# Kernel tuning notes

Hardware: AMD Instinct MI355X
Metric: run time of the kernel (lower is better)

The kernel has to match this reference:

```python
import jax, jax.numpy as jnp
import numpy as np

SEQDIM = 512      # hidden-state dim of h
EMBED_DIM = 512   # attention embedding dim
VFEAT_DIM = 384   # visual feature channels (must equal VFEAT_LEN for the broadcast in the original code)
VFEAT_LEN = 384   # number of visual regions


def setup_inputs() -> dict:
    key = jax.random.key(0)
    k_h, k_v, k_wh, k_wv, k_wg = jax.random.split(key, 5)
    h = jax.random.normal(k_h, (SEQDIM, 1), dtype=jnp.float32)
    v = jax.random.normal(k_v, (VFEAT_DIM, VFEAT_LEN), dtype=jnp.float32)
    wh = jax.random.normal(k_wh, (VFEAT_LEN, EMBED_DIM), dtype=jnp.float32) * 0.05
    wv = jax.random.normal(k_wv, (EMBED_DIM, VFEAT_DIM), dtype=jnp.float32) * 0.05
    wg = jax.random.normal(k_wg, (EMBED_DIM, SEQDIM), dtype=jnp.float32) * 0.05
    return {"h": h, "v": v, "wh": wh, "wv": wv, "wg": wg}


def reference(h, v, wh, wv, wg):
    # s = W_v V + (W_g h_t) 1^T  -> (embed_dim, vfeat_len)
    s = jnp.matmul(wv, v) + jnp.matmul(wg, h)  # (E, L) + (E, 1) broadcasts == outer product with ones row
    # z = w_h tanh(s)            -> (vfeat_len, vfeat_len)
    z = jnp.matmul(wh, jnp.tanh(s))
    alpha = jax.nn.softmax(z, axis=-1)
    # v (D, L) * alpha[..., None] (L, L, 1) -> broadcast to (L, D, L) with D == L
    weighted_avg = v * alpha[..., None]
    return weighted_avg
```

## Files before the change

kernel.cpp:

```cpp
#include <hip/hip_runtime.h>
#include <hip/hip_bf16.h>

#define SDIM 512
#define EDIM 512
#define LDIM 384
#define DDIM 384

typedef __attribute__((ext_vector_type(4))) float float4v;

__global__ __launch_bounds__(256) void k_tanh_s(
    const float* __restrict__ h, const float* __restrict__ v,
    const float* __restrict__ wv, const float* __restrict__ wg,
    float* __restrict__ t)
{
    const int e0  = blockIdx.x * 2;
    const int tid = threadIdx.x;
    __shared__ float wvs[2 * DDIM];
    __shared__ float red[2][2];

    {
        const int row  = tid >> 7;
        const int l128 = tid & 127;
        float acc = 0.f;
        for (int k = l128; k < SDIM; k += 128)
            acc += wg[(e0 + row) * SDIM + k] * h[k];
        for (int off = 32; off > 0; off >>= 1)
            acc += __shfl_down(acc, off, 64);
        if ((tid & 63) == 0) red[row][(tid >> 6) & 1] = acc;
    }

    for (int k = tid; k < 2 * DDIM; k += 256)
        wvs[k] = wv[e0 * DDIM + k];
    __syncthreads();

    const float gh0 = red[0][0] + red[0][1];
    const float gh1 = red[1][0] + red[1][1];

    for (int l = tid; l < LDIM; l += 256) {
        float a0 = 0.f, a1 = 0.f, b0 = 0.f, b1 = 0.f;
        const float* vp = v + l;
        #pragma unroll 8
        for (int k = 0; k < DDIM; k += 2) {
            const float v0 = vp[k * LDIM];
            const float v1 = vp[(k + 1) * LDIM];
            a0 += wvs[k]        * v0;
            a1 += wvs[k + 1]    * v1;
            b0 += wvs[DDIM + k]     * v0;
            b1 += wvs[DDIM + k + 1] * v1;
        }
        t[e0 * LDIM + l]       = tanhf((a0 + a1) + gh0);
        t[(e0 + 1) * LDIM + l] = tanhf((b0 + b1) + gh1);
    }
}

__global__ __launch_bounds__(256) void k_softmax(
    const float* __restrict__ wh, const float* __restrict__ t,
    float* __restrict__ alpha)
{
    const int r0  = blockIdx.x * 2;
    const int tid = threadIdx.x;
    __shared__ float whs[2 * EDIM];
    __shared__ float zr[2][LDIM];
    __shared__ float redm[2][2];
    __shared__ float reds[2][2];

    for (int e = tid; e < 2 * EDIM; e += 256)
        whs[e] = wh[r0 * EDIM + e];
    __syncthreads();

    for (int c = tid; c < LDIM; c += 256) {
        float z00 = 0.f, z01 = 0.f, z10 = 0.f, z11 = 0.f;
        #pragma unroll 8
        for (int e = 0; e < EDIM; e += 2) {
            const float t0 = t[e * LDIM + c];
            const float t1 = t[(e + 1) * LDIM + c];
            z00 += whs[e]     * t0;
            z01 += whs[e + 1] * t1;
            z10 += whs[EDIM + e]     * t0;
            z11 += whs[EDIM + e + 1] * t1;
        }
        zr[0][c] = z00 + z01;
        zr[1][c] = z10 + z11;
    }
    __syncthreads();

    const int row = tid >> 7;
    const int l1  = tid & 127;

    float m = -INFINITY;
    for (int c = l1; c < LDIM; c += 128) m = fmaxf(m, zr[row][c]);
    for (int off = 32; off > 0; off >>= 1)
        m = fmaxf(m, __shfl_down(m, off, 64));
    if ((tid & 63) == 0) redm[row][(tid >> 6) & 1] = m;
    __syncthreads();
    m = fmaxf(redm[row][0], redm[row][1]);

    float sum = 0.f;
    for (int c = l1; c < LDIM; c += 128) {
        const float ez = expf(zr[row][c] - m);
        zr[row][c] = ez;
        sum += ez;
    }
    for (int off = 32; off > 0; off >>= 1)
        sum += __shfl_down(sum, off, 64);
    if ((tid & 63) == 0) reds[row][(tid >> 6) & 1] = sum;
    __syncthreads();
    const float rs = 1.f / (reds[row][0] + reds[row][1]);

    for (int c = l1; c < LDIM; c += 128)
        alpha[(r0 + row) * LDIM + c] = zr[row][c] * rs;
}

__global__ __launch_bounds__(256) void k_out(
    const float* __restrict__ v, const float* __restrict__ alpha,
    float* __restrict__ out)
{
    constexpr int VPS  = (LDIM * DDIM) / 4;
    constexpr int HALF = VPS / 2;
    const int i = blockIdx.x >> 1;
    const int h = blockIdx.x & 1;

    __shared__ float arow[DDIM];
    for (int j = threadIdx.x; j < DDIM; j += 256)
        arow[j] = alpha[i * DDIM + j];
    __syncthreads();

    const float4v* v4 = (const float4v*)v;
    float4v* o4 = (float4v*)out + (size_t)i * VPS;
    const int base = h * HALF;

    #pragma unroll 4
    for (int it = 0; it < HALF / 256; ++it) {
        const int idx = base + it * 256 + (int)threadIdx.x;
        const int j   = idx / 96;
        const float a = arow[j];
        float4v vv = v4[idx];
        vv *= a;
        __builtin_nontemporal_store(vv, o4 + idx);
    }
}

extern "C" void kernel_launch(void* const* d_in, const int* in_sizes, int n_in,
                              void* d_out, int out_size, void* d_ws, size_t ws_size,
                              hipStream_t stream)
{
    const float* h  = (const float*)d_in[0];
    const float* v  = (const float*)d_in[1];
    const float* wh = (const float*)d_in[2];
    const float* wv = (const float*)d_in[3];
    const float* wg = (const float*)d_in[4];
    float* out = (float*)d_out;

    float* t     = (float*)d_ws;
    float* alpha = t + EDIM * LDIM;

    k_tanh_s <<<EDIM / 2, 256, 0, stream>>>(h, v, wv, wg, t);
    k_softmax<<<LDIM / 2, 256, 0, stream>>>(wh, t, alpha);
    k_out    <<<2 * LDIM, 256, 0, stream>>>(v, alpha, out);
}
```

Before: 300.3 us.

## Remap matvec kernels to one row per block with 384 threads

Both matvec kernels now launch one block per output row with 384 threads, one thread per column. This replaces the old two-rows-per-block, 256-thread layout, which left half the threads idle in the second column pass. The softmax now runs straight from registers without a shared row buffer. The output kernel is split into quarters so it launches more blocks. The cost is that each block now reuses every loaded v/t column for only one row instead of two, which doubles global reads of those matrices.

```diff
diff --git a/kernel.cpp b/kernel.cpp
--- a/kernel.cpp
+++ b/kernel.cpp
@@ -8,117 +8,94 @@
 
 typedef __attribute__((ext_vector_type(4))) float float4v;
 
-__global__ __launch_bounds__(256) void k_tanh_s(
+__global__ __launch_bounds__(384) void k_tanh_s(
     const float* __restrict__ h, const float* __restrict__ v,
     const float* __restrict__ wv, const float* __restrict__ wg,
     float* __restrict__ t)
 {
-    const int e0  = blockIdx.x * 2;
+    const int e   = blockIdx.x;
     const int tid = threadIdx.x;
-    __shared__ float wvs[2 * DDIM];
-    __shared__ float red[2][2];
+    __shared__ float wvs[DDIM];
+    __shared__ float red[6];
 
-    {
-        const int row  = tid >> 7;
-        const int l128 = tid & 127;
-        float acc = 0.f;
-        for (int k = l128; k < SDIM; k += 128)
-            acc += wg[(e0 + row) * SDIM + k] * h[k];
-        for (int off = 32; off > 0; off >>= 1)
-            acc += __shfl_down(acc, off, 64);
-        if ((tid & 63) == 0) red[row][(tid >> 6) & 1] = acc;
-    }
+    float acc = 0.f;
+    for (int k = tid; k < SDIM; k += 384)
+        acc += wg[e * SDIM + k] * h[k];
+    for (int off = 32; off > 0; off >>= 1)
+        acc += __shfl_down(acc, off, 64);
+    if ((tid & 63) == 0) red[tid >> 6] = acc;
 
-    for (int k = tid; k < 2 * DDIM; k += 256)
-        wvs[k] = wv[e0 * DDIM + k];
+    wvs[tid] = wv[e * DDIM + tid];
     __syncthreads();
 
-    const float gh0 = red[0][0] + red[0][1];
-    const float gh1 = red[1][0] + red[1][1];
+    const float gh = red[0] + red[1] + red[2] + red[3] + red[4] + red[5];
 
-    for (int l = tid; l < LDIM; l += 256) {
-        float a0 = 0.f, a1 = 0.f, b0 = 0.f, b1 = 0.f;
-        const float* vp = v + l;
-        #pragma unroll 8
-        for (int k = 0; k < DDIM; k += 2) {
-            const float v0 = vp[k * LDIM];
-            const float v1 = vp[(k + 1) * LDIM];
-            a0 += wvs[k]        * v0;
-            a1 += wvs[k + 1]    * v1;
-            b0 += wvs[DDIM + k]     * v0;
-            b1 += wvs[DDIM + k + 1] * v1;
-        }
-        t[e0 * LDIM + l]       = tanhf((a0 + a1) + gh0);
-        t[(e0 + 1) * LDIM + l] = tanhf((b0 + b1) + gh1);
+    const float* vp = v + tid;
+    float a0 = 0.f, a1 = 0.f, a2 = 0.f, a3 = 0.f;
+    #pragma unroll 4
+    for (int k = 0; k < DDIM; k += 4) {
+        a0 += wvs[k]     * vp[(k)     * LDIM];
+        a1 += wvs[k + 1] * vp[(k + 1) * LDIM];
+        a2 += wvs[k + 2] * vp[(k + 2) * LDIM];
+        a3 += wvs[k + 3] * vp[(k + 3) * LDIM];
     }
+    t[e * LDIM + tid] = tanhf((a0 + a1) + (a2 + a3) + gh);
 }
 
-__global__ __launch_bounds__(256) void k_softmax(
+__global__ __launch_bounds__(384) void k_softmax(
     const float* __restrict__ wh, const float* __restrict__ t,
     float* __restrict__ alpha)
 {
-    const int r0  = blockIdx.x * 2;
+    const int r   = blockIdx.x;
     const int tid = threadIdx.x;
-    __shared__ float whs[2 * EDIM];
-    __shared__ float zr[2][LDIM];
-    __shared__ float redm[2][2];
-    __shared__ float reds[2][2];
+    __shared__ float whs[EDIM];
+    __shared__ float redm[6];
+    __shared__ float reds[6];
 
-    for (int e = tid; e < 2 * EDIM; e += 256)
-        whs[e] = wh[r0 * EDIM + e];
+    for (int e = tid; e < EDIM; e += 384)
+        whs[e] = wh[r * EDIM + e];
     __syncthreads();
 
-    for (int c = tid; c < LDIM; c += 256) {
-        float z00 = 0.f, z01 = 0.f, z10 = 0.f, z11 = 0.f;
-        #pragma unroll 8
-        for (int e = 0; e < EDIM; e += 2) {
-            const float t0 = t[e * LDIM + c];
-            const float t1 = t[(e + 1) * LDIM + c];
-            z00 += whs[e]     * t0;
-            z01 += whs[e + 1] * t1;
-            z10 += whs[EDIM + e]     * t0;
-            z11 += whs[EDIM + e + 1] * t1;
-        }
-        zr[0][c] = z00 + z01;
-        zr[1][c] = z10 + z11;
+    const float* tp = t + tid;
+    float a0 = 0.f, a1 = 0.f, a2 = 0.f, a3 = 0.f;
+    #pragma unroll 4
+    for (int e = 0; e < EDIM; e += 4) {
+        a0 += whs[e]     * tp[(e)     * LDIM];
+        a1 += whs[e + 1] * tp[(e + 1) * LDIM];
+        a2 += whs[e + 2] * tp[(e + 2) * LDIM];
+        a3 += whs[e + 3] * tp[(e + 3) * LDIM];
     }
-    __syncthreads();
+    const float z = (a0 + a1) + (a2 + a3);
 
-    const int row = tid >> 7;
-    const int l1  = tid & 127;
-
-    float m = -INFINITY;
-    for (int c = l1; c < LDIM; c += 128) m = fmaxf(m, zr[row][c]);
+    float m = z;
     for (int off = 32; off > 0; off >>= 1)
         m = fmaxf(m, __shfl_down(m, off, 64));
-    if ((tid & 63) == 0) redm[row][(tid >> 6) & 1] = m;
+    if ((tid & 63) == 0) redm[tid >> 6] = m;
     __syncthreads();
-    m = fmaxf(redm[row][0], redm[row][1]);
+    m = fmaxf(fmaxf(fmaxf(redm[0], redm[1]), fmaxf(redm[2], redm[3])),
+              fmaxf(redm[4], redm[5]));
 
-    float sum = 0.f;
-    for (int c = l1; c < LDIM; c += 128) {
-        const float ez = expf(zr[row][c] - m);
-        zr[row][c] = ez;
-        sum += ez;
-    }
+    const float ez = expf(z - m);
+
+    float s = ez;
     for (int off = 32; off > 0; off >>= 1)
-        sum += __shfl_down(sum, off, 64);
-    if ((tid & 63) == 0) reds[row][(tid >> 6) & 1] = sum;
+        s += __shfl_down(s, off, 64);
+    if ((tid & 63) == 0) reds[tid >> 6] = s;
     __syncthreads();
-    const float rs = 1.f / (reds[row][0] + reds[row][1]);
+    const float rs = 1.f / (((reds[0] + reds[1]) + (reds[2] + reds[3]))
+                            + (reds[4] + reds[5]));
 
-    for (int c = l1; c < LDIM; c += 128)
-        alpha[(r0 + row) * LDIM + c] = zr[row][c] * rs;
+    alpha[r * LDIM + tid] = ez * rs;
 }
 
 __global__ __launch_bounds__(256) void k_out(
     const float* __restrict__ v, const float* __restrict__ alpha,
     float* __restrict__ out)
 {
-    constexpr int VPS  = (LDIM * DDIM) / 4;
-    constexpr int HALF = VPS / 2;
-    const int i = blockIdx.x >> 1;
-    const int h = blockIdx.x & 1;
+    constexpr int VPS = (LDIM * DDIM) / 4;
+    constexpr int QTR = VPS / 4;
+    const int i = blockIdx.x >> 2;
+    const int q = blockIdx.x & 3;
 
     __shared__ float arow[DDIM];
     for (int j = threadIdx.x; j < DDIM; j += 256)
@@ -127,10 +104,10 @@
 
     const float4v* v4 = (const float4v*)v;
     float4v* o4 = (float4v*)out + (size_t)i * VPS;
-    const int base = h * HALF;
+    const int base = q * QTR;
 
     #pragma unroll 4
-    for (int it = 0; it < HALF / 256; ++it) {
+    for (int it = 0; it < QTR / 256; ++it) {
         const int idx = base + it * 256 + (int)threadIdx.x;
         const int j   = idx / 96;
         const float a = arow[j];
@@ -154,7 +131,7 @@
     float* t     = (float*)d_ws;
     float* alpha = t + EDIM * LDIM;
 
-    k_tanh_s <<<EDIM / 2, 256, 0, stream>>>(h, v, wv, wg, t);
-    k_softmax<<<LDIM / 2, 256, 0, stream>>>(wh, t, alpha);
-    k_out    <<<2 * LDIM, 256, 0, stream>>>(v, alpha, out);
+    k_tanh_s <<<EDIM, 384, 0, stream>>>(h, v, wv, wg, t);
+    k_softmax<<<LDIM, 384, 0, stream>>>(wh, t, alpha);
+    k_out    <<<4 * LDIM, 256, 0, stream>>>(v, alpha, out);
 }
```

Result: faster. 274.6 us (-8.6%).
